# Performance work log

Hardware: AMD Instinct MI355X
Metric: run time of the kernel (lower is better)

Reference implementation:

```python
import jax, jax.numpy as jnp
import numpy as np

B, N, C, HEADS, SR = 4, 16384, 64, 2, 8
SIDE = 128            # sqrt(N)
NKV = (SIDE // SR) ** 2  # 256
D = C // HEADS
LN_EPS = 1e-5


def setup_inputs() -> dict:
    key = jax.random.key(0)
    ks = jax.random.split(key, 12)
    s = 0.02
    return {
        "x": jax.random.normal(ks[0], (B, N, C), jnp.float32),
        "pos_2D": jax.random.uniform(ks[1], (B, HEADS, N, NKV), jnp.float32),
        "q_w": jax.random.normal(ks[2], (C, C), jnp.float32) * s,
        "q_b": jnp.zeros((C,), jnp.float32),
        "kv_w": jax.random.normal(ks[3], (2 * C, C), jnp.float32) * s,
        "kv_b": jnp.zeros((2 * C,), jnp.float32),
        "proj_w": jax.random.normal(ks[4], (C, C), jnp.float32) * s,
        "proj_b": jnp.zeros((C,), jnp.float32),
        "sr_w": jax.random.normal(ks[5], (C, C, SR, SR), jnp.float32) * s,  # OIHW
        "sr_b": jnp.zeros((C,), jnp.float32),
        "ln_g": jnp.ones((C,), jnp.float32),
        "ln_b": jnp.zeros((C,), jnp.float32),
        "alpha": jnp.full((1,), 0.3, jnp.float32),
    }


def reference(x, pos_2D, q_w, q_b, kv_w, kv_b, proj_w, proj_b, sr_w, sr_b, ln_g, ln_b, alpha):
    scale = D ** -0.5
    # q projection -> [B, HEADS, N, D]
    q = (jnp.einsum("bnc,oc->bno", x, q_w) + q_b).reshape(B, N, HEADS, D).transpose(0, 2, 1, 3)
    # spatial reduction: conv stride SR on [B, C, SIDE, SIDE]
    xs = x.transpose(0, 2, 1).reshape(B, C, SIDE, SIDE)
    xs = jax.lax.conv_general_dilated(
        xs, sr_w, window_strides=(SR, SR), padding="VALID",
        dimension_numbers=("NCHW", "OIHW", "NCHW")) + sr_b[None, :, None, None]
    xs = xs.reshape(B, C, NKV).transpose(0, 2, 1)  # [B, NKV, C]
    # LayerNorm over channels
    mu = jnp.mean(xs, axis=-1, keepdims=True)
    var = jnp.mean(jnp.square(xs - mu), axis=-1, keepdims=True)
    xs = (xs - mu) * jax.lax.rsqrt(var + LN_EPS) * ln_g + ln_b
    # kv projection -> k, v each [B, HEADS, NKV, D]
    kv = (jnp.einsum("bmc,oc->bmo", xs, kv_w) + kv_b).reshape(B, NKV, 2, HEADS, D)
    kv = kv.transpose(2, 0, 3, 1, 4)
    k, v = kv[0], kv[1]
    # attention with post-softmax positional blend
    attn = jax.nn.softmax(jnp.einsum("bhnd,bhmd->bhnm", q, k) * scale, axis=-1)
    a = alpha[0]
    attn = (1.0 - a) * attn + a * pos_2D
    out = jnp.einsum("bhnm,bhmd->bhnd", attn, v)
    out = out.transpose(0, 2, 1, 3).reshape(B, N, C)
    return jnp.einsum("bnc,oc->bno", out, proj_w) + proj_b
```

## Files before the change

### kernel.cpp

```cpp
#include <hip/hip_runtime.h>
#include <cstdint>
#include <cstddef>

#define NN 16384
#define CC 64
#define LN_EPS 1e-5f

typedef __attribute__((ext_vector_type(8))) short short8;
typedef __attribute__((ext_vector_type(4))) float f32x4;
typedef unsigned short ushort_t;
typedef unsigned int uint32;

__device__ __forceinline__ ushort_t f2bf(float f) {
  union { float f; uint32 u; } v; v.f = f;
  return (ushort_t)((v.u + 0x8000u) >> 16);
}
__device__ __forceinline__ uint32 pk2(float a, float b) {
  union { float f; uint32 u; } x, y; x.f = a; y.f = b;
  return ((x.u + 0x8000u) >> 16) | ((y.u + 0x8000u) & 0xffff0000u);
}
__device__ __forceinline__ short8 pk8(float4 a, float4 b) {
  union { short8 s; uint32 u[4]; } r;
  r.u[0] = pk2(a.x, a.y); r.u[1] = pk2(a.z, a.w);
  r.u[2] = pk2(b.x, b.y); r.u[3] = pk2(b.z, b.w);
  return r.s;
}

__global__ __launch_bounds__(256) void qproj_prep_kernel(const float* __restrict__ x,
    const float* __restrict__ q_w, const float* __restrict__ q_b,
    const float* __restrict__ sr_w, ushort_t* __restrict__ q_out, ushort_t* __restrict__ w3) {
  __shared__ __align__(16) ushort_t q_tile[64*64];
  int t = threadIdx.x;
  {
    int e = blockIdx.x*256 + t;
    int kh = e >> 15, rem = e & 32767, o = rem >> 9, kp = rem & 511;
    int kw = kp >> 6, i = kp & 63;
    w3[e] = f2bf(sr_w[o*4096 + i*64 + kh*8 + kw]);
  }
  int w = t >> 6, lane = t & 63;
  int quad = lane >> 4, col = lane & 15;
  const float qscale = 0.17677669529663687f * 1.4426950408889634f;
  short8 bfr[4][2];
  float qb[4];
  #pragma unroll
  for (int ct = 0; ct < 4; ++ct) {
    #pragma unroll
    for (int ksb = 0; ksb < 2; ++ksb) {
      const float* src = &q_w[(ct*16 + col)*64 + ksb*32 + quad*8];
      bfr[ct][ksb] = pk8(*(const float4*)src, *(const float4*)(src + 4));
    }
    qb[ct] = q_b[ct*16 + col];
  }
  int rows0 = blockIdx.x*64;
  int arow = rows0 + w*16 + col;
  const float* xs = &x[(size_t)arow*64];
  short8 af0 = pk8(*(const float4*)&xs[quad*8],      *(const float4*)&xs[quad*8 + 4]);
  short8 af1 = pk8(*(const float4*)&xs[32 + quad*8], *(const float4*)&xs[36 + quad*8]);
  const f32x4 zero = {0.f, 0.f, 0.f, 0.f};
  #pragma unroll
  for (int ct = 0; ct < 4; ++ct) {
    f32x4 acc = __builtin_amdgcn_mfma_f32_16x16x32_bf16(af0, bfr[ct][0], zero, 0, 0, 0);
    acc = __builtin_amdgcn_mfma_f32_16x16x32_bf16(af1, bfr[ct][1], acc, 0, 0, 0);
    #pragma unroll
    for (int r = 0; r < 4; ++r)
      q_tile[(w*16 + quad*4 + r)*64 + ct*16 + col] = f2bf((acc[r] + qb[ct]) * qscale);
  }
  __syncthreads();
  int u = t;
  #pragma unroll
  for (int s = 0; s < 2; ++s, u += 256) {
    int row = u >> 3, seg = u & 7;
    int h2 = seg >> 2, sg = seg & 3;
    uint4 val = *(const uint4*)&q_tile[row*64 + seg*8];
    int gr = rows0 + row;
    int b2 = gr >> 14, n = gr & 16383;
    *(uint4*)&q_out[((size_t)(b2*2 + h2)*NN + n)*32 + sg*8] = val;
  }
}

__global__ __launch_bounds__(256) void conv_kernel(const float* __restrict__ x,
                                                   const ushort_t* __restrict__ w3,
                                                   float* __restrict__ part) {
  __shared__ __align__(16) ushort_t A_lds[32*520];
  __shared__ __align__(16) ushort_t W_lds[64*520];
  int t = threadIdx.x;
  int pt = blockIdx.x >> 3, kc = blockIdx.x & 7;
  {
    const uint4* src = (const uint4*)&w3[kc*32768];
    #pragma unroll
    for (int v = 0; v < 16; ++v) {
      int g = v*256 + t;
      int o = g >> 6, off8 = (g & 63)*8;
      *(uint4*)&W_lds[o*520 + off8] = src[g];
    }
  }
  #pragma unroll
  for (int v = 0; v < 8; ++v) {
    int g = v*256 + t;
    int pl = g >> 6, off8 = (g & 63)*8;
    int p = pt*32 + pl;
    int b = p >> 8, ph = (p >> 4) & 15, pw = p & 15;
    int n0 = (ph*8 + kc)*128 + pw*8;
    const float* src = &x[((size_t)b*NN + n0)*64 + off8];
    *(short8*)&A_lds[pl*520 + off8] = pk8(*(const float4*)src, *(const float4*)(src + 4));
  }
  __syncthreads();
  int w = t >> 6, lane = t & 63, quad = lane >> 4, col = lane & 15;
  int mt = w & 1, nh = w >> 1;
  const ushort_t* Ab = &A_lds[(mt*16 + col)*520 + quad*8];
  const ushort_t* Bb = &W_lds[(nh*32 + col)*520 + quad*8];
  const f32x4 zero = {0.f, 0.f, 0.f, 0.f};
  f32x4 acc0 = zero, acc1 = zero;
  #pragma unroll
  for (int ks = 0; ks < 16; ++ks) {
    short8 af = *(const short8*)(Ab + ks*32);
    short8 b0 = *(const short8*)(Bb + ks*32);
    short8 b1 = *(const short8*)(Bb + 16*520 + ks*32);
    acc0 = __builtin_amdgcn_mfma_f32_16x16x32_bf16(af, b0, acc0, 0, 0, 0);
    acc1 = __builtin_amdgcn_mfma_f32_16x16x32_bf16(af, b1, acc1, 0, 0, 0);
  }
  #pragma unroll
  for (int r = 0; r < 4; ++r) {
    int p = pt*32 + mt*16 + quad*4 + r;
    part[((kc << 10) + p)*64 + nh*32 + col]      = acc0[r];
    part[((kc << 10) + p)*64 + nh*32 + 16 + col] = acc1[r];
  }
}

__global__ __launch_bounds__(256) void lnkv_kernel(const float* __restrict__ part,
    const float* __restrict__ sr_b, const float* __restrict__ ln_g, const float* __restrict__ ln_b,
    const float* __restrict__ kv_w, const float* __restrict__ kv_b,
    ushort_t* __restrict__ k_out, ushort_t* __restrict__ v_out) {
  __shared__ float xsrow[4][64];
  int t = threadIdx.x;
  int w = t >> 6, lane = t & 63;
  float4 wk[16], wv[16];
  #pragma unroll
  for (int c4 = 0; c4 < 16; ++c4) {
    wk[c4] = *(const float4*)&kv_w[lane*64 + c4*4];
    wv[c4] = *(const float4*)&kv_w[(64+lane)*64 + c4*4];
  }
  float kb0 = kv_b[lane], kb1 = kv_b[64+lane];
  float sb = sr_b[lane], lg = ln_g[lane], lb = ln_b[lane];
  int h = lane >> 5, dd = lane & 31;
  for (int i = 0; i < 2; ++i) {
    int row = blockIdx.x*8 + w*2 + i;
    float xc = sb;
    #pragma unroll
    for (int kc = 0; kc < 8; ++kc) xc += part[kc*65536 + row*64 + lane];
    float s = xc;
    #pragma unroll
    for (int m = 1; m < 64; m <<= 1) s += __shfl_xor(s, m);
    float mu = s * (1.0f/64.0f);
    float d0 = xc - mu;
    float vs = d0*d0;
    #pragma unroll
    for (int m = 1; m < 64; m <<= 1) vs += __shfl_xor(vs, m);
    float rs = rsqrtf(vs*(1.0f/64.0f) + LN_EPS);
    xsrow[w][lane] = d0*rs*lg + lb;
    float acc0 = kb0, acc1 = kb1;
    #pragma unroll
    for (int c4 = 0; c4 < 16; ++c4) {
      float4 xv = *(const float4*)&xsrow[w][c4*4];
      acc0 += xv.x*wk[c4].x + xv.y*wk[c4].y + xv.z*wk[c4].z + xv.w*wk[c4].w;
      acc1 += xv.x*wv[c4].x + xv.y*wv[c4].y + xv.z*wv[c4].z + xv.w*wv[c4].w;
    }
    int b = row >> 8, m2 = row & 255;
    int bh = b*2 + h;
    k_out[(bh*256 + m2)*32 + dd] = f2bf(acc0);
    v_out[(bh*32 + dd)*256 + m2] = f2bf(acc1);
  }
}

__global__ __launch_bounds__(256, 2) void attn_kernel(const ushort_t* __restrict__ q_ws,
    const ushort_t* __restrict__ k_ws, const ushort_t* __restrict__ v_ws,
    const float* __restrict__ pos, const float* __restrict__ alpha,
    ushort_t* __restrict__ attnout) {
  __shared__ __align__(16) ushort_t k_lds[256*40];
  __shared__ __align__(16) ushort_t v_lds[32*264];
  __shared__ __align__(16) ushort_t p_lds[4][16*264];
  int t = threadIdx.x;
  int bh = blockIdx.x >> 6, blk = blockIdx.x & 63;
  {
    const uint4* ksrc = (const uint4*)(k_ws + bh*8192);
    const uint4* vsrc = (const uint4*)(v_ws + bh*8192);
    uint4* kd = (uint4*)k_lds; uint4* vd = (uint4*)v_lds;
    #pragma unroll
    for (int vv = 0; vv < 4; ++vv) {
      int i = t + vv*256;
      kd[(i >> 2)*5 + (i & 3)] = ksrc[i];
      vd[(i >> 5)*33 + (i & 31)] = vsrc[i];
    }
  }
  __syncthreads();
  int w = t >> 6, lane = t & 63, quad = lane >> 4, col = lane & 15;
  float a = alpha[0];
  float one_minus_a = 1.0f - a;
  const f32x4 zero = {0.f, 0.f, 0.f, 0.f};
  for (int it = 0; it < 4; ++it) {
    int n0 = blk*256 + (it*4 + w)*16;
    float4 p4[16];
    const float* pbase = &pos[((size_t)bh*NN + n0 + col)*256 + quad*8];
    #pragma unroll
    for (int ks = 0; ks < 8; ++ks) {
      p4[ks*2]   = *(const float4*)(pbase + ks*32);
      p4[ks*2+1] = *(const float4*)(pbase + ks*32 + 4);
    }
    short8 qa = *(const short8*)&q_ws[((size_t)bh*NN + n0 + col)*32 + quad*8];
    f32x4 st[16];
    #pragma unroll
    for (int tt = 0; tt < 16; ++tt) {
      short8 kb = *(const short8*)&k_lds[(tt*16 + col)*40 + quad*8];
      st[tt] = __builtin_amdgcn_mfma_f32_16x16x32_bf16(kb, qa, zero, 0, 0, 0);
    }
    float sum = 0.f;
    #pragma unroll
    for (int tt = 0; tt < 16; ++tt) {
      #pragma unroll
      for (int r = 0; r < 4; ++r) {
        float e = __builtin_amdgcn_exp2f(st[tt][r]);
        st[tt][r] = e; sum += e;
      }
    }
    sum += __shfl_xor(sum, 16);
    sum += __shfl_xor(sum, 32);
    float coef = one_minus_a * __builtin_amdgcn_rcpf(sum);
    #pragma unroll
    for (int tt = 0; tt < 16; ++tt) {
      uint2 val = { pk2(st[tt][0], st[tt][1]), pk2(st[tt][2], st[tt][3]) };
      *(uint2*)&p_lds[w][col*264 + tt*16 + quad*4] = val;
    }
    f32x4 o0 = zero, o1 = zero, e0 = zero, e1 = zero;
    #pragma unroll
    for (int ks = 0; ks < 8; ++ks) {
      short8 pa  = *(const short8*)&p_lds[w][col*264 + ks*32 + quad*8];
      short8 vb0 = *(const short8*)&v_lds[(col)*264 + ks*32 + quad*8];
      short8 vb1 = *(const short8*)&v_lds[(16 + col)*264 + ks*32 + quad*8];
      short8 pf  = pk8(p4[ks*2], p4[ks*2+1]);
      o0 = __builtin_amdgcn_mfma_f32_16x16x32_bf16(vb0, pa, o0, 0, 0, 0);
      o1 = __builtin_amdgcn_mfma_f32_16x16x32_bf16(vb1, pa, o1, 0, 0, 0);
      e0 = __builtin_amdgcn_mfma_f32_16x16x32_bf16(vb0, pf, e0, 0, 0, 0);
      e1 = __builtin_amdgcn_mfma_f32_16x16x32_bf16(vb1, pf, e1, 0, 0, 0);
    }
    ushort_t* obase = &attnout[((size_t)bh*NN + n0 + col)*32];
    uint2 v0 = { pk2(coef*o0[0] + a*e0[0], coef*o0[1] + a*e0[1]),
                 pk2(coef*o0[2] + a*e0[2], coef*o0[3] + a*e0[3]) };
    uint2 v1 = { pk2(coef*o1[0] + a*e1[0], coef*o1[1] + a*e1[1]),
                 pk2(coef*o1[2] + a*e1[2], coef*o1[3] + a*e1[3]) };
    *(uint2*)&obase[quad*4]      = v0;
    *(uint2*)&obase[16 + quad*4] = v1;
  }
}

__global__ __launch_bounds__(256) void proj_kernel(const ushort_t* __restrict__ attnout,
    const float* __restrict__ proj_w, const float* __restrict__ proj_b, float* __restrict__ out) {
  __shared__ __align__(16) float o_tile[64*68];
  int t = threadIdx.x;
  int w = t >> 6, lane = t & 63;
  int quad = lane >> 4, col = lane & 15;
  short8 bfr[4][2];
  float pb[4];
  #pragma unroll
  for (int ct = 0; ct < 4; ++ct) {
    #pragma unroll
    for (int ksb = 0; ksb < 2; ++ksb) {
      const float* src = &proj_w[(ct*16 + col)*64 + ksb*32 + quad*8];
      bfr[ct][ksb] = pk8(*(const float4*)src, *(const float4*)(src + 4));
    }
    pb[ct] = proj_b[ct*16 + col];
  }
  int rows0 = blockIdx.x*64;
  int arow = rows0 + w*16 + col;
  int b2 = arow >> 14, n = arow & 16383;
  short8 af0 = *(const short8*)&attnout[((size_t)(b2*2)*NN + n)*32 + quad*8];
  short8 af1 = *(const short8*)&attnout[((size_t)(b2*2 + 1)*NN + n)*32 + quad*8];
  const f32x4 zero = {0.f, 0.f, 0.f, 0.f};
  #pragma unroll
  for (int ct = 0; ct < 4; ++ct) {
    f32x4 acc = __builtin_amdgcn_mfma_f32_16x16x32_bf16(af0, bfr[ct][0], zero, 0, 0, 0);
    acc = __builtin_amdgcn_mfma_f32_16x16x32_bf16(af1, bfr[ct][1], acc, 0, 0, 0);
    #pragma unroll
    for (int r = 0; r < 4; ++r)
      o_tile[(w*16 + quad*4 + r)*68 + ct*16 + col] = acc[r] + pb[ct];
  }
  __syncthreads();
  int u = t;
  #pragma unroll
  for (int s = 0; s < 4; ++s, u += 256) {
    int row = u >> 4, c4 = u & 15;
    float4 val = *(const float4*)&o_tile[row*68 + c4*4];
    *(float4*)&out[(size_t)(rows0 + row)*64 + c4*4] = val;
  }
}

extern "C" void kernel_launch(void* const* d_in, const int* in_sizes, int n_in,
                              void* d_out, int out_size, void* d_ws, size_t ws_size,
                              hipStream_t stream) {
  const float* x      = (const float*)d_in[0];
  const float* pos    = (const float*)d_in[1];
  const float* q_w    = (const float*)d_in[2];
  const float* q_b    = (const float*)d_in[3];
  const float* kv_w   = (const float*)d_in[4];
  const float* kv_b   = (const float*)d_in[5];
  const float* proj_w = (const float*)d_in[6];
  const float* proj_b = (const float*)d_in[7];
  const float* sr_w   = (const float*)d_in[8];
  const float* sr_b   = (const float*)d_in[9];
  const float* ln_g   = (const float*)d_in[10];
  const float* ln_b   = (const float*)d_in[11];
  const float* alpha  = (const float*)d_in[12];
  float* out = (float*)d_out;

  char* ws = (char*)d_ws;
  float* part       = (float*)(ws);
  ushort_t* w3      = (ushort_t*)(ws + (2u<<20));
  ushort_t* k_ws    = (ushort_t*)(ws + (3u<<20));
  ushort_t* v_ws    = (ushort_t*)(ws + (3u<<20) + (128u<<10));
  ushort_t* q_ws    = (ushort_t*)(ws + (4u<<20));
  ushort_t* a_ws    = (ushort_t*)(ws + (12u<<20));

  hipLaunchKernelGGL(qproj_prep_kernel, dim3(1024), dim3(256), 0, stream, x, q_w, q_b, sr_w, q_ws, w3);
  hipLaunchKernelGGL(conv_kernel,       dim3(256),  dim3(256), 0, stream, x, w3, part);
  hipLaunchKernelGGL(lnkv_kernel,       dim3(128),  dim3(256), 0, stream, part, sr_b, ln_g, ln_b, kv_w, kv_b, k_ws, v_ws);
  hipLaunchKernelGGL(attn_kernel,       dim3(512),  dim3(256), 0, stream, q_ws, k_ws, v_ws, pos, alpha, a_ws);
  hipLaunchKernelGGL(proj_kernel,       dim3(1024), dim3(256), 0, stream, a_ws, proj_w, proj_b, out);
}
```

Baseline: 261.4 us.

## Fuse conv into q-projection pass and fold output projection into attention

Splits the weight reformat into its own prep kernel and merges the strided conv with the q-projection, so each block reads one image row of x once for both. The attention kernel now processes both heads per block and applies the output projection in-register via an LDS staging tile, which removes the bf16 attention-output round trip and the separate proj kernel. K and V are now read straight from global or cache instead of staged in LDS. Grid size for attention halves to 256 blocks, which lowers parallelism and lengthens the serial work in each block.

```diff
diff --git a/kernel.cpp b/kernel.cpp
--- a/kernel.cpp
+++ b/kernel.cpp
@@ -26,19 +26,33 @@
   return r.s;
 }
 
-__global__ __launch_bounds__(256) void qproj_prep_kernel(const float* __restrict__ x,
+__global__ void prep_kernel(const float* __restrict__ sr_w, ushort_t* __restrict__ w3) {
+  int e = blockIdx.x*256 + threadIdx.x;
+  int kh = e >> 15, rem = e & 32767, o = rem >> 9, kp = rem & 511;
+  int kw = kp >> 6, i = kp & 63;
+  w3[e] = f2bf(sr_w[o*4096 + i*64 + kh*8 + kw]);
+}
+
+__global__ __launch_bounds__(256) void stage1_kernel(const float* __restrict__ x,
     const float* __restrict__ q_w, const float* __restrict__ q_b,
-    const float* __restrict__ sr_w, ushort_t* __restrict__ q_out, ushort_t* __restrict__ w3) {
-  __shared__ __align__(16) ushort_t q_tile[64*64];
+    const ushort_t* __restrict__ w3, ushort_t* __restrict__ q_out, float* __restrict__ part) {
+  __shared__ __align__(16) ushort_t x_tile[16*520];
+  __shared__ __align__(16) ushort_t q_tile[128*64];
   int t = threadIdx.x;
-  {
-    int e = blockIdx.x*256 + t;
-    int kh = e >> 15, rem = e & 32767, o = rem >> 9, kp = rem & 511;
-    int kw = kp >> 6, i = kp & 63;
-    w3[e] = f2bf(sr_w[o*4096 + i*64 + kh*8 + kw]);
-  }
-  int w = t >> 6, lane = t & 63;
-  int quad = lane >> 4, col = lane & 15;
+  int g = blockIdx.x;
+  int b = g >> 7;
+  int r_img = g & 127;
+  int kh = r_img & 7, ph = r_img >> 3;
+  size_t gr0 = (size_t)g * 128;
+  const float* xblk = &x[gr0*64];
+  #pragma unroll
+  for (int v = 0; v < 4; ++v) {
+    int e8 = v*256 + t;
+    int pw = e8 >> 6, kp8 = (e8 & 63)*8;
+    const float* s = xblk + e8*8;
+    *(short8*)&x_tile[pw*520 + kp8] = pk8(*(const float4*)s, *(const float4*)(s + 4));
+  }
+  int w = t >> 6, lane = t & 63, quad = lane >> 4, col = lane & 15;
   const float qscale = 0.17677669529663687f * 1.4426950408889634f;
   short8 bfr[4][2];
   float qb[4];
@@ -51,79 +65,47 @@
     }
     qb[ct] = q_b[ct*16 + col];
   }
-  int rows0 = blockIdx.x*64;
-  int arow = rows0 + w*16 + col;
-  const float* xs = &x[(size_t)arow*64];
-  short8 af0 = pk8(*(const float4*)&xs[quad*8],      *(const float4*)&xs[quad*8 + 4]);
-  short8 af1 = pk8(*(const float4*)&xs[32 + quad*8], *(const float4*)&xs[36 + quad*8]);
   const f32x4 zero = {0.f, 0.f, 0.f, 0.f};
   #pragma unroll
-  for (int ct = 0; ct < 4; ++ct) {
-    f32x4 acc = __builtin_amdgcn_mfma_f32_16x16x32_bf16(af0, bfr[ct][0], zero, 0, 0, 0);
-    acc = __builtin_amdgcn_mfma_f32_16x16x32_bf16(af1, bfr[ct][1], acc, 0, 0, 0);
-    #pragma unroll
-    for (int r = 0; r < 4; ++r)
-      q_tile[(w*16 + quad*4 + r)*64 + ct*16 + col] = f2bf((acc[r] + qb[ct]) * qscale);
+  for (int mt = 0; mt < 2; ++mt) {
+    int row = w*32 + mt*16 + col;
+    const float* xs = xblk + row*64;
+    short8 af0 = pk8(*(const float4*)&xs[quad*8],      *(const float4*)&xs[quad*8 + 4]);
+    short8 af1 = pk8(*(const float4*)&xs[32 + quad*8], *(const float4*)&xs[36 + quad*8]);
+    #pragma unroll
+    for (int ct = 0; ct < 4; ++ct) {
+      f32x4 acc = __builtin_amdgcn_mfma_f32_16x16x32_bf16(af0, bfr[ct][0], zero, 0, 0, 0);
+      acc = __builtin_amdgcn_mfma_f32_16x16x32_bf16(af1, bfr[ct][1], acc, 0, 0, 0);
+      #pragma unroll
+      for (int r = 0; r < 4; ++r)
+        q_tile[(w*32 + mt*16 + quad*4 + r)*64 + ct*16 + col] = f2bf((acc[r] + qb[ct]) * qscale);
+    }
   }
   __syncthreads();
-  int u = t;
-  #pragma unroll
-  for (int s = 0; s < 2; ++s, u += 256) {
+  {
+    const ushort_t* wbase = &w3[kh*32768 + (w*16 + col)*512 + quad*8];
+    const ushort_t* abase = &x_tile[col*520 + quad*8];
+    f32x4 acc = zero;
+    #pragma unroll
+    for (int ks = 0; ks < 16; ++ks) {
+      short8 af = *(const short8*)(abase + ks*32);
+      short8 bf = *(const short8*)(wbase + ks*32);
+      acc = __builtin_amdgcn_mfma_f32_16x16x32_bf16(af, bf, acc, 0, 0, 0);
+    }
+    #pragma unroll
+    for (int r = 0; r < 4; ++r) {
+      int p = b*256 + ph*16 + quad*4 + r;
+      part[kh*65536 + p*64 + w*16 + col] = acc[r];
+    }
+  }
+  #pragma unroll
+  for (int s = 0; s < 4; ++s) {
+    int u = s*256 + t;
     int row = u >> 3, seg = u & 7;
     int h2 = seg >> 2, sg = seg & 3;
     uint4 val = *(const uint4*)&q_tile[row*64 + seg*8];
-    int gr = rows0 + row;
-    int b2 = gr >> 14, n = gr & 16383;
-    *(uint4*)&q_out[((size_t)(b2*2 + h2)*NN + n)*32 + sg*8] = val;
-  }
-}
-
-__global__ __launch_bounds__(256) void conv_kernel(const float* __restrict__ x,
-                                                   const ushort_t* __restrict__ w3,
-                                                   float* __restrict__ part) {
-  __shared__ __align__(16) ushort_t A_lds[32*520];
-  __shared__ __align__(16) ushort_t W_lds[64*520];
-  int t = threadIdx.x;
-  int pt = blockIdx.x >> 3, kc = blockIdx.x & 7;
-  {
-    const uint4* src = (const uint4*)&w3[kc*32768];
-    #pragma unroll
-    for (int v = 0; v < 16; ++v) {
-      int g = v*256 + t;
-      int o = g >> 6, off8 = (g & 63)*8;
-      *(uint4*)&W_lds[o*520 + off8] = src[g];
-    }
-  }
-  #pragma unroll
-  for (int v = 0; v < 8; ++v) {
-    int g = v*256 + t;
-    int pl = g >> 6, off8 = (g & 63)*8;
-    int p = pt*32 + pl;
-    int b = p >> 8, ph = (p >> 4) & 15, pw = p & 15;
-    int n0 = (ph*8 + kc)*128 + pw*8;
-    const float* src = &x[((size_t)b*NN + n0)*64 + off8];
-    *(short8*)&A_lds[pl*520 + off8] = pk8(*(const float4*)src, *(const float4*)(src + 4));
-  }
-  __syncthreads();
-  int w = t >> 6, lane = t & 63, quad = lane >> 4, col = lane & 15;
-  int mt = w & 1, nh = w >> 1;
-  const ushort_t* Ab = &A_lds[(mt*16 + col)*520 + quad*8];
-  const ushort_t* Bb = &W_lds[(nh*32 + col)*520 + quad*8];
-  const f32x4 zero = {0.f, 0.f, 0.f, 0.f};
-  f32x4 acc0 = zero, acc1 = zero;
-  #pragma unroll
-  for (int ks = 0; ks < 16; ++ks) {
-    short8 af = *(const short8*)(Ab + ks*32);
-    short8 b0 = *(const short8*)(Bb + ks*32);
-    short8 b1 = *(const short8*)(Bb + 16*520 + ks*32);
-    acc0 = __builtin_amdgcn_mfma_f32_16x16x32_bf16(af, b0, acc0, 0, 0, 0);
-    acc1 = __builtin_amdgcn_mfma_f32_16x16x32_bf16(af, b1, acc1, 0, 0, 0);
-  }
-  #pragma unroll
-  for (int r = 0; r < 4; ++r) {
-    int p = pt*32 + mt*16 + quad*4 + r;
-    part[((kc << 10) + p)*64 + nh*32 + col]      = acc0[r];
-    part[((kc << 10) + p)*64 + nh*32 + 16 + col] = acc1[r];
+    int n = r_img*128 + row;
+    *(uint4*)&q_out[((size_t)(b*2 + h2)*NN + n)*32 + sg*8] = val;
   }
 }
 
@@ -172,124 +154,93 @@
   }
 }
 
-__global__ __launch_bounds__(256, 2) void attn_kernel(const ushort_t* __restrict__ q_ws,
+__global__ __launch_bounds__(256, 2) void attn2_kernel(const ushort_t* __restrict__ q_ws,
     const ushort_t* __restrict__ k_ws, const ushort_t* __restrict__ v_ws,
     const float* __restrict__ pos, const float* __restrict__ alpha,
-    ushort_t* __restrict__ attnout) {
-  __shared__ __align__(16) ushort_t k_lds[256*40];
-  __shared__ __align__(16) ushort_t v_lds[32*264];
+    const float* __restrict__ proj_w, const float* __restrict__ proj_b,
+    float* __restrict__ out) {
   __shared__ __align__(16) ushort_t p_lds[4][16*264];
+  __shared__ __align__(16) ushort_t o_lds[4][16*72];
   int t = threadIdx.x;
-  int bh = blockIdx.x >> 6, blk = blockIdx.x & 63;
-  {
-    const uint4* ksrc = (const uint4*)(k_ws + bh*8192);
-    const uint4* vsrc = (const uint4*)(v_ws + bh*8192);
-    uint4* kd = (uint4*)k_lds; uint4* vd = (uint4*)v_lds;
-    #pragma unroll
-    for (int vv = 0; vv < 4; ++vv) {
-      int i = t + vv*256;
-      kd[(i >> 2)*5 + (i & 3)] = ksrc[i];
-      vd[(i >> 5)*33 + (i & 31)] = vsrc[i];
-    }
-  }
-  __syncthreads();
+  int b = blockIdx.x >> 6, blk = blockIdx.x & 63;
   int w = t >> 6, lane = t & 63, quad = lane >> 4, col = lane & 15;
   float a = alpha[0];
   float one_minus_a = 1.0f - a;
+  short8 pwf[4][2];
+  #pragma unroll
+  for (int ct = 0; ct < 4; ++ct) {
+    #pragma unroll
+    for (int ks2 = 0; ks2 < 2; ++ks2) {
+      const float* src = &proj_w[(ct*16 + col)*64 + ks2*32 + quad*8];
+      pwf[ct][ks2] = pk8(*(const float4*)src, *(const float4*)(src + 4));
+    }
+  }
   const f32x4 zero = {0.f, 0.f, 0.f, 0.f};
   for (int it = 0; it < 4; ++it) {
     int n0 = blk*256 + (it*4 + w)*16;
-    float4 p4[16];
-    const float* pbase = &pos[((size_t)bh*NN + n0 + col)*256 + quad*8];
-    #pragma unroll
-    for (int ks = 0; ks < 8; ++ks) {
-      p4[ks*2]   = *(const float4*)(pbase + ks*32);
-      p4[ks*2+1] = *(const float4*)(pbase + ks*32 + 4);
-    }
-    short8 qa = *(const short8*)&q_ws[((size_t)bh*NN + n0 + col)*32 + quad*8];
-    f32x4 st[16];
-    #pragma unroll
-    for (int tt = 0; tt < 16; ++tt) {
-      short8 kb = *(const short8*)&k_lds[(tt*16 + col)*40 + quad*8];
-      st[tt] = __builtin_amdgcn_mfma_f32_16x16x32_bf16(kb, qa, zero, 0, 0, 0);
-    }
-    float sum = 0.f;
-    #pragma unroll
-    for (int tt = 0; tt < 16; ++tt) {
-      #pragma unroll
-      for (int r = 0; r < 4; ++r) {
-        float e = __builtin_amdgcn_exp2f(st[tt][r]);
-        st[tt][r] = e; sum += e;
-      }
-    }
-    sum += __shfl_xor(sum, 16);
-    sum += __shfl_xor(sum, 32);
-    float coef = one_minus_a * __builtin_amdgcn_rcpf(sum);
-    #pragma unroll
-    for (int tt = 0; tt < 16; ++tt) {
-      uint2 val = { pk2(st[tt][0], st[tt][1]), pk2(st[tt][2], st[tt][3]) };
-      *(uint2*)&p_lds[w][col*264 + tt*16 + quad*4] = val;
-    }
-    f32x4 o0 = zero, o1 = zero, e0 = zero, e1 = zero;
-    #pragma unroll
-    for (int ks = 0; ks < 8; ++ks) {
-      short8 pa  = *(const short8*)&p_lds[w][col*264 + ks*32 + quad*8];
-      short8 vb0 = *(const short8*)&v_lds[(col)*264 + ks*32 + quad*8];
-      short8 vb1 = *(const short8*)&v_lds[(16 + col)*264 + ks*32 + quad*8];
-      short8 pf  = pk8(p4[ks*2], p4[ks*2+1]);
-      o0 = __builtin_amdgcn_mfma_f32_16x16x32_bf16(vb0, pa, o0, 0, 0, 0);
-      o1 = __builtin_amdgcn_mfma_f32_16x16x32_bf16(vb1, pa, o1, 0, 0, 0);
-      e0 = __builtin_amdgcn_mfma_f32_16x16x32_bf16(vb0, pf, e0, 0, 0, 0);
-      e1 = __builtin_amdgcn_mfma_f32_16x16x32_bf16(vb1, pf, e1, 0, 0, 0);
-    }
-    ushort_t* obase = &attnout[((size_t)bh*NN + n0 + col)*32];
-    uint2 v0 = { pk2(coef*o0[0] + a*e0[0], coef*o0[1] + a*e0[1]),
-                 pk2(coef*o0[2] + a*e0[2], coef*o0[3] + a*e0[3]) };
-    uint2 v1 = { pk2(coef*o1[0] + a*e1[0], coef*o1[1] + a*e1[1]),
-                 pk2(coef*o1[2] + a*e1[2], coef*o1[3] + a*e1[3]) };
-    *(uint2*)&obase[quad*4]      = v0;
-    *(uint2*)&obase[16 + quad*4] = v1;
-  }
-}
-
-__global__ __launch_bounds__(256) void proj_kernel(const ushort_t* __restrict__ attnout,
-    const float* __restrict__ proj_w, const float* __restrict__ proj_b, float* __restrict__ out) {
-  __shared__ __align__(16) float o_tile[64*68];
-  int t = threadIdx.x;
-  int w = t >> 6, lane = t & 63;
-  int quad = lane >> 4, col = lane & 15;
-  short8 bfr[4][2];
-  float pb[4];
-  #pragma unroll
-  for (int ct = 0; ct < 4; ++ct) {
-    #pragma unroll
-    for (int ksb = 0; ksb < 2; ++ksb) {
-      const float* src = &proj_w[(ct*16 + col)*64 + ksb*32 + quad*8];
-      bfr[ct][ksb] = pk8(*(const float4*)src, *(const float4*)(src + 4));
-    }
-    pb[ct] = proj_b[ct*16 + col];
-  }
-  int rows0 = blockIdx.x*64;
-  int arow = rows0 + w*16 + col;
-  int b2 = arow >> 14, n = arow & 16383;
-  short8 af0 = *(const short8*)&attnout[((size_t)(b2*2)*NN + n)*32 + quad*8];
-  short8 af1 = *(const short8*)&attnout[((size_t)(b2*2 + 1)*NN + n)*32 + quad*8];
-  const f32x4 zero = {0.f, 0.f, 0.f, 0.f};
-  #pragma unroll
-  for (int ct = 0; ct < 4; ++ct) {
-    f32x4 acc = __builtin_amdgcn_mfma_f32_16x16x32_bf16(af0, bfr[ct][0], zero, 0, 0, 0);
-    acc = __builtin_amdgcn_mfma_f32_16x16x32_bf16(af1, bfr[ct][1], acc, 0, 0, 0);
-    #pragma unroll
-    for (int r = 0; r < 4; ++r)
-      o_tile[(w*16 + quad*4 + r)*68 + ct*16 + col] = acc[r] + pb[ct];
-  }
-  __syncthreads();
-  int u = t;
-  #pragma unroll
-  for (int s = 0; s < 4; ++s, u += 256) {
-    int row = u >> 4, c4 = u & 15;
-    float4 val = *(const float4*)&o_tile[row*68 + c4*4];
-    *(float4*)&out[(size_t)(rows0 + row)*64 + c4*4] = val;
+    #pragma unroll
+    for (int h = 0; h < 2; ++h) {
+      int bh = b*2 + h;
+      float4 p4[16];
+      const float* pbase = &pos[((size_t)bh*NN + n0 + col)*256 + quad*8];
+      #pragma unroll
+      for (int ks = 0; ks < 8; ++ks) {
+        p4[ks*2]   = *(const float4*)(pbase + ks*32);
+        p4[ks*2+1] = *(const float4*)(pbase + ks*32 + 4);
+      }
+      short8 qa = *(const short8*)&q_ws[((size_t)bh*NN + n0 + col)*32 + quad*8];
+      f32x4 st[16];
+      #pragma unroll
+      for (int tt = 0; tt < 16; ++tt) {
+        short8 kb = *(const short8*)&k_ws[((size_t)bh*256 + tt*16 + col)*32 + quad*8];
+        st[tt] = __builtin_amdgcn_mfma_f32_16x16x32_bf16(kb, qa, zero, 0, 0, 0);
+      }
+      float sum = 0.f;
+      #pragma unroll
+      for (int tt = 0; tt < 16; ++tt) {
+        #pragma unroll
+        for (int r = 0; r < 4; ++r) {
+          float e = __builtin_amdgcn_exp2f(st[tt][r]);
+          st[tt][r] = e; sum += e;
+        }
+      }
+      sum += __shfl_xor(sum, 16);
+      sum += __shfl_xor(sum, 32);
+      float coef = one_minus_a * __builtin_amdgcn_rcpf(sum);
+      #pragma unroll
+      for (int tt = 0; tt < 16; ++tt) {
+        uint2 val = { pk2(st[tt][0], st[tt][1]), pk2(st[tt][2], st[tt][3]) };
+        *(uint2*)&p_lds[w][col*264 + tt*16 + quad*4] = val;
+      }
+      f32x4 o0 = zero, o1 = zero, e0 = zero, e1 = zero;
+      #pragma unroll
+      for (int ks = 0; ks < 8; ++ks) {
+        short8 pa  = *(const short8*)&p_lds[w][col*264 + ks*32 + quad*8];
+        short8 vb0 = *(const short8*)&v_ws[((size_t)bh*32 + col)*256 + ks*32 + quad*8];
+        short8 vb1 = *(const short8*)&v_ws[((size_t)bh*32 + 16 + col)*256 + ks*32 + quad*8];
+        short8 pf  = pk8(p4[ks*2], p4[ks*2+1]);
+        o0 = __builtin_amdgcn_mfma_f32_16x16x32_bf16(vb0, pa, o0, 0, 0, 0);
+        o1 = __builtin_amdgcn_mfma_f32_16x16x32_bf16(vb1, pa, o1, 0, 0, 0);
+        e0 = __builtin_amdgcn_mfma_f32_16x16x32_bf16(vb0, pf, e0, 0, 0, 0);
+        e1 = __builtin_amdgcn_mfma_f32_16x16x32_bf16(vb1, pf, e1, 0, 0, 0);
+      }
+      uint2 u0 = { pk2(coef*o0[0] + a*e0[0], coef*o0[1] + a*e0[1]),
+                   pk2(coef*o0[2] + a*e0[2], coef*o0[3] + a*e0[3]) };
+      uint2 u1 = { pk2(coef*o1[0] + a*e1[0], coef*o1[1] + a*e1[1]),
+                   pk2(coef*o1[2] + a*e1[2], coef*o1[3] + a*e1[3]) };
+      *(uint2*)&o_lds[w][col*72 + h*32 + quad*4]      = u0;
+      *(uint2*)&o_lds[w][col*72 + h*32 + 16 + quad*4] = u1;
+    }
+    short8 ob0 = *(const short8*)&o_lds[w][col*72 + quad*8];
+    short8 ob1 = *(const short8*)&o_lds[w][col*72 + 32 + quad*8];
+    #pragma unroll
+    for (int ct = 0; ct < 4; ++ct) {
+      f32x4 acc = __builtin_amdgcn_mfma_f32_16x16x32_bf16(pwf[ct][0], ob0, zero, 0, 0, 0);
+      acc = __builtin_amdgcn_mfma_f32_16x16x32_bf16(pwf[ct][1], ob1, acc, 0, 0, 0);
+      float4 pbv = *(const float4*)&proj_b[ct*16 + quad*4];
+      float4 res = { acc[0] + pbv.x, acc[1] + pbv.y, acc[2] + pbv.z, acc[3] + pbv.w };
+      *(float4*)&out[((size_t)b*NN + n0 + col)*64 + ct*16 + quad*4] = res;
+    }
   }
 }
 
@@ -317,11 +268,9 @@
   ushort_t* k_ws    = (ushort_t*)(ws + (3u<<20));
   ushort_t* v_ws    = (ushort_t*)(ws + (3u<<20) + (128u<<10));
   ushort_t* q_ws    = (ushort_t*)(ws + (4u<<20));
-  ushort_t* a_ws    = (ushort_t*)(ws + (12u<<20));
-
-  hipLaunchKernelGGL(qproj_prep_kernel, dim3(1024), dim3(256), 0, stream, x, q_w, q_b, sr_w, q_ws, w3);
-  hipLaunchKernelGGL(conv_kernel,       dim3(256),  dim3(256), 0, stream, x, w3, part);
-  hipLaunchKernelGGL(lnkv_kernel,       dim3(128),  dim3(256), 0, stream, part, sr_b, ln_g, ln_b, kv_w, kv_b, k_ws, v_ws);
-  hipLaunchKernelGGL(attn_kernel,       dim3(512),  dim3(256), 0, stream, q_ws, k_ws, v_ws, pos, alpha, a_ws);
-  hipLaunchKernelGGL(proj_kernel,       dim3(1024), dim3(256), 0, stream, a_ws, proj_w, proj_b, out);
-}
+
+  hipLaunchKernelGGL(prep_kernel,   dim3(1024), dim3(256), 0, stream, sr_w, w3);
+  hipLaunchKernelGGL(stage1_kernel, dim3(512),  dim3(256), 0, stream, x, q_w, q_b, w3, q_ws, part);
+  hipLaunchKernelGGL(lnkv_kernel,   dim3(128),  dim3(256), 0, stream, part, sr_b, ln_g, ln_b, kv_w, kv_b, k_ws, v_ws);
+  hipLaunchKernelGGL(attn2_kernel,  dim3(256),  dim3(256), 0, stream, q_ws, k_ws, v_ws, pos, alpha, proj_w, proj_b, out);
+}
```

After: 323.7 us. +23.8%, slower.
